# Kernel tuning notes

Measured on AMD Instinct MI355X. Metric: run time of the kernel, lower is better.

## Reference

```python
import jax, jax.numpy as jnp
import numpy as np

N = 200_000        # nodes
E = 2_000_000      # edges (before self loops)
D = 128            # emb_dim
L = 5              # num_layer
NUM_ATOM = 120     # num_atom_type
NUM_CHI = 3        # num_chirality_tag
NUM_BOND = 6       # num_bond_type
NUM_DIR = 3        # num_bond_direction
EPS = 1e-5


def setup_inputs() -> dict:
    key = jax.random.key(0)
    ks = jax.random.split(key, 12)
    s = 0.1
    return {
        "x": jax.random.randint(ks[0], (N, 2), 0, 3, dtype=jnp.int64) if jax.config.jax_enable_x64 else jax.random.randint(ks[0], (N, 2), 0, 3, dtype=jnp.int32),
        "edge_index": jax.random.randint(ks[1], (2, E), 0, N, dtype=jnp.int32),
        "edge_attr": jax.random.randint(ks[2], (E, 2), 0, 3, dtype=jnp.int32),
        "x_emb1": jax.random.normal(ks[3], (NUM_ATOM, D), jnp.float32) * s,
        "x_emb2": jax.random.normal(ks[4], (NUM_CHI, D), jnp.float32) * s,
        "edge_emb1": jax.random.normal(ks[5], (L, NUM_BOND, D), jnp.float32) * s,
        "edge_emb2": jax.random.normal(ks[6], (L, NUM_DIR, D), jnp.float32) * s,
        "w1": jax.random.normal(ks[7], (L, D, 2 * D), jnp.float32) * s,
        "b1": jnp.zeros((L, 2 * D), jnp.float32),
        "w2": jax.random.normal(ks[8], (L, 2 * D, D), jnp.float32) * s,
        "b2": jnp.zeros((L, D), jnp.float32),
        "bn_gamma": jnp.ones((L, D), jnp.float32),
        "bn_beta": jnp.zeros((L, D), jnp.float32),
    }


def reference(x, edge_index, edge_attr, x_emb1, x_emb2, edge_emb1, edge_emb2,
              w1, b1, w2, b2, bn_gamma, bn_beta):
    # node features: atom-type emb + chirality emb
    h = x_emb1[x[:, 0]] + x_emb2[x[:, 1]]                     # [N, D]

    # add self loops; self-loop edge_attr = [4, 0]
    loop = jnp.arange(N, dtype=edge_index.dtype)
    src = jnp.concatenate([edge_index[0], loop])              # [E+N]
    dst = jnp.concatenate([edge_index[1], loop])              # [E+N]
    ea0 = jnp.concatenate([edge_attr[:, 0], jnp.full((N,), 4, edge_attr.dtype)])
    ea1 = jnp.concatenate([edge_attr[:, 1], jnp.zeros((N,), edge_attr.dtype)])

    for l in range(L):
        e_emb = edge_emb1[l][ea0] + edge_emb2[l][ea1]         # [E+N, D]
        msg = h[src] + e_emb                                  # gather + add
        agg = jax.ops.segment_sum(msg, dst, num_segments=N)   # scatter-add
        hid = jax.nn.relu(agg @ w1[l] + b1[l])                # [N, 2D]
        hn = hid @ w2[l] + b2[l]                              # [N, D]
        # BatchNorm1d (training mode, biased variance)
        mean = hn.mean(axis=0)
        var = jnp.mean((hn - mean) ** 2, axis=0)
        hn = bn_gamma[l] * (hn - mean) * jax.lax.rsqrt(var + EPS) + bn_beta[l]
        if l < L - 1:
            hn = jax.nn.relu(hn)
        h = hn
    return h
```

## Files before the change

kernel.cpp:

```cpp
#include <hip/hip_runtime.h>

#define NN 200000
#define NPAD 200192
#define NE 2000000
#define DD 128
#define EPSF 1e-5f

typedef short short4v __attribute__((ext_vector_type(4)));
typedef short short8v __attribute__((ext_vector_type(8)));
typedef float f32x4 __attribute__((ext_vector_type(4)));
typedef float f32x2 __attribute__((ext_vector_type(2)));
typedef unsigned long long u64;

__device__ __forceinline__ ushort f2bf(float f) {
  uint u = __float_as_uint(f);
  uint r = u + 0x7fff + ((u >> 16) & 1);
  return (ushort)(r >> 16);
}
__device__ __forceinline__ float bf2f(ushort u) { return __uint_as_float(((uint)u) << 16); }
__device__ __forceinline__ float bflo(uint v) { return __uint_as_float(v << 16); }
__device__ __forceinline__ float bfhi(uint v) { return __uint_as_float(v & 0xffff0000u); }
__device__ __forceinline__ uint packbf(float a, float b) {
  return (uint)f2bf(a) | ((uint)f2bf(b) << 16);
}

__global__ __launch_bounds__(256) void k_init(const int* __restrict__ x,
    const float* __restrict__ e1, const float* __restrict__ e2,
    uint* __restrict__ h) {
  int t = blockIdx.x * 256 + threadIdx.x;
  if (t >= NN * 64) return;
  int node = t >> 6, cp = (t & 63) << 1;
  int a = x[2 * node], b = x[2 * node + 1];
  float2 va = *(const float2*)(e1 + (size_t)a * DD + cp);
  float2 vb = *(const float2*)(e2 + (size_t)b * DD + cp);
  h[t] = packbf(va.x + vb.x, va.y + vb.y);
}

__global__ __launch_bounds__(256) void k_cvtw(const float* __restrict__ w,
    ushort* __restrict__ wt, int K, int Nc) {
  int t = blockIdx.x * 256 + threadIdx.x;
  if (t >= 5 * K * Nc) return;
  int per = K * Nc;
  int l = t / per, r0 = t % per;
  int j = r0 & 7, lane = (r0 >> 3) & 63, idx = r0 >> 9;
  int KB = K >> 5;
  int kb = idx % KB, ct = idx / KB;
  int lr = lane & 15, qq = lane >> 4;
  int n = ct * 16 + lr;
  int k = kb * 32 + qq * 4 + (j & 3) + ((j >> 2) << 4);
  wt[t] = f2bf(w[(size_t)l * per + (size_t)k * Nc + n]);
}

__global__ __launch_bounds__(256) void k_hist(const int* __restrict__ ei,
    const int* __restrict__ ea, u64* __restrict__ hist8) {
  int e = blockIdx.x * 256 + threadIdx.x;
  if (e >= NE) return;
  int d = ei[NE + e];
  int a0 = ea[2 * e];
  int a1 = ea[2 * e + 1];
  u64 v = (1ull << (a0 * 10)) | (1ull << (30 + a1 * 10));
  atomicAdd(&hist8[(size_t)(blockIdx.x & 7) * NN + d], v);
}

__global__ __launch_bounds__(256) void k_scan1(const u64* __restrict__ hist8,
    u64* __restrict__ histsum, int* __restrict__ off, int* __restrict__ bsum) {
  __shared__ int sh[256];
  int i = blockIdx.x * 256 + threadIdx.x;
  int v = 0;
  if (i < NN) {
    u64 s = 0;
#pragma unroll
    for (int cc = 0; cc < 8; ++cc) s += hist8[(size_t)cc * NN + i];
    histsum[i] = s;
    v = (int)((s & 1023) + ((s >> 10) & 1023) + ((s >> 20) & 1023));
  }
  sh[threadIdx.x] = v;
  __syncthreads();
  for (int d = 1; d < 256; d <<= 1) {
    int xv = 0;
    if (threadIdx.x >= d) xv = sh[threadIdx.x - d];
    __syncthreads();
    if (threadIdx.x >= d) sh[threadIdx.x] += xv;
    __syncthreads();
  }
  if (i < NN) off[i] = sh[threadIdx.x] - v;
  if (threadIdx.x == 255) bsum[blockIdx.x] = sh[255];
}

__global__ __launch_bounds__(1024) void k_scan2(const int* __restrict__ bsum,
    int* __restrict__ boff, int nb) {
  __shared__ int sh[1024];
  int t = threadIdx.x;
  int v = (t < nb) ? bsum[t] : 0;
  sh[t] = v;
  __syncthreads();
  for (int d = 1; d < 1024; d <<= 1) {
    int xv = 0;
    if (t >= d) xv = sh[t - d];
    __syncthreads();
    if (t >= d) sh[t] += xv;
    __syncthreads();
  }
  if (t < nb) boff[t] = sh[t] - v;
}

__global__ __launch_bounds__(256) void k_scan3(int* __restrict__ off,
    const int* __restrict__ boff, const u64* __restrict__ hist8,
    int* __restrict__ cursor8) {
  int i = blockIdx.x * 256 + threadIdx.x;
  if (i < NN) {
    int o = off[i] + boff[i >> 8];
    off[i] = o;
    int run = o;
#pragma unroll
    for (int s = 0; s < 8; ++s) {
      cursor8[(size_t)s * NN + i] = run;
      u64 hs = hist8[(size_t)s * NN + i];
      run += (int)((hs & 1023) + ((hs >> 10) & 1023) + ((hs >> 20) & 1023));
    }
  }
  if (i == 0) off[NN] = NE;
}

__global__ __launch_bounds__(256) void k_scatter(const int* __restrict__ ei,
    int* __restrict__ cursor8, int* __restrict__ csr_src) {
  int e = blockIdx.x * 256 + threadIdx.x;
  if (e >= NE) return;
  int d = ei[NE + e];
  int p = atomicAdd(&cursor8[(size_t)(blockIdx.x & 7) * NN + d], 1);
  csr_src[p] = ei[e];
}

__global__ __launch_bounds__(256) void k_agg(const uint* __restrict__ h,
    uint* __restrict__ agghi, uint* __restrict__ agglo,
    const int* __restrict__ off, const int* __restrict__ src,
    const u64* __restrict__ hist,
    const float* __restrict__ E1, const float* __restrict__ E2) {
  int lane = threadIdx.x & 63;
  int node = blockIdx.x * 4 + (threadIdx.x >> 6);
  int qq = lane >> 4;
  int c = lane & 15;
  f32x2 acc[4];
#pragma unroll
  for (int j = 0; j < 4; ++j) acc[j] = (f32x2){0.f, 0.f};

#define ACCV(V)                                                           \
  {                                                                       \
    acc[0] += (f32x2){bflo(V.x), bfhi(V.x)};                              \
    acc[1] += (f32x2){bflo(V.y), bfhi(V.y)};                              \
    acc[2] += (f32x2){bflo(V.z), bfhi(V.z)};                              \
    acc[3] += (f32x2){bflo(V.w), bfhi(V.w)};                              \
  }

  int beg = off[node], end = off[node + 1];
  int deg = end - beg;
  for (int base = 0; base < deg; base += 64) {
    int nrem = min(deg - base, 64);
    int myidx = 0;
    if (lane < nrem) myidx = src[beg + base + lane];
    int niter = (nrem + 3) >> 2;
    for (int m = 0; m < niter; m += 4) {
      int sl0 = qq + 4 * m;
      int sl1 = sl0 + 4, sl2 = sl0 + 8, sl3 = sl0 + 12;
      int s0 = __shfl(myidx, min(sl0, nrem - 1));
      int s1 = __shfl(myidx, min(sl1, nrem - 1));
      int s2 = __shfl(myidx, min(sl2, nrem - 1));
      int s3 = __shfl(myidx, min(sl3, nrem - 1));
      uint4 v0 = *(const uint4*)(h + (size_t)s0 * 64 + c * 4);
      if (sl0 < nrem) ACCV(v0);
      if (m + 1 < niter) {
        uint4 v1 = *(const uint4*)(h + (size_t)s1 * 64 + c * 4);
        if (sl1 < nrem) ACCV(v1);
      }
      if (m + 2 < niter) {
        uint4 v2 = *(const uint4*)(h + (size_t)s2 * 64 + c * 4);
        if (sl2 < nrem) ACCV(v2);
      }
      if (m + 3 < niter) {
        uint4 v3 = *(const uint4*)(h + (size_t)s3 * 64 + c * 4);
        if (sl3 < nrem) ACCV(v3);
      }
    }
  }
#pragma unroll
  for (int j = 0; j < 4; ++j) {
    acc[j][0] += __shfl_xor(acc[j][0], 16);
    acc[j][1] += __shfl_xor(acc[j][1], 16);
    acc[j][0] += __shfl_xor(acc[j][0], 32);
    acc[j][1] += __shfl_xor(acc[j][1], 32);
  }
  if (lane < 16) {
    uint4 sv = *(const uint4*)(h + (size_t)node * 64 + c * 4);
    ACCV(sv);
    float a[8];
#pragma unroll
    for (int j = 0; j < 4; ++j) { a[2 * j] = acc[j][0]; a[2 * j + 1] = acc[j][1]; }
    u64 hv = hist[node];
    float cnt[7] = {
      (float)(int)(hv & 1023),
      (float)(int)((hv >> 10) & 1023),
      (float)(int)((hv >> 20) & 1023),
      1.f,
      (float)(int)((hv >> 30) & 1023) + 1.f,
      (float)(int)((hv >> 40) & 1023),
      (float)(int)((hv >> 50) & 1023)
    };
    const float* rows[7] = {E1, E1 + DD, E1 + 2 * DD, E1 + 4 * DD,
                            E2, E2 + DD, E2 + 2 * DD};
#pragma unroll
    for (int q = 0; q < 7; ++q) {
      f32x4 e0 = *(const f32x4*)(rows[q] + c * 8);
      f32x4 e1v = *(const f32x4*)(rows[q] + c * 8 + 4);
#pragma unroll
      for (int j = 0; j < 4; ++j) { a[j] += cnt[q] * e0[j]; a[4 + j] += cnt[q] * e1v[j]; }
    }
    int wb = ((c >> 2) << 4) + ((c & 1) << 3) + (((c >> 1) & 1) << 1);
    ushort hA, hB;
    uint2 w01, w23, l01, l23;
    hA = f2bf(a[0]); hB = f2bf(a[1]);
    w01.x = (uint)hA | ((uint)hB << 16);
    l01.x = (uint)f2bf(a[0] - bf2f(hA)) | ((uint)f2bf(a[1] - bf2f(hB)) << 16);
    hA = f2bf(a[2]); hB = f2bf(a[3]);
    w01.y = (uint)hA | ((uint)hB << 16);
    l01.y = (uint)f2bf(a[2] - bf2f(hA)) | ((uint)f2bf(a[3] - bf2f(hB)) << 16);
    hA = f2bf(a[4]); hB = f2bf(a[5]);
    w23.x = (uint)hA | ((uint)hB << 16);
    l23.x = (uint)f2bf(a[4] - bf2f(hA)) | ((uint)f2bf(a[5] - bf2f(hB)) << 16);
    hA = f2bf(a[6]); hB = f2bf(a[7]);
    w23.y = (uint)hA | ((uint)hB << 16);
    l23.y = (uint)f2bf(a[6] - bf2f(hA)) | ((uint)f2bf(a[7] - bf2f(hB)) << 16);
    *(uint2*)(agghi + (size_t)node * 64 + wb) = w01;
    *(uint2*)(agghi + (size_t)node * 64 + wb + 4) = w23;
    *(uint2*)(agglo + (size_t)node * 64 + wb) = l01;
    *(uint2*)(agglo + (size_t)node * 64 + wb + 4) = l23;
  }
#undef ACCV
}

__global__ __launch_bounds__(512, 1) void k_mlp(
    const ushort* __restrict__ agghi, const ushort* __restrict__ agglo,
    const ushort* __restrict__ w1,
    const float* __restrict__ b1,
    const ushort* __restrict__ w2,
    const float* __restrict__ b2, uint* __restrict__ hnb,
    float* __restrict__ bnsums) {
  __shared__ uint4 smem4[8192];
  __shared__ float sstat[256];
  const ushort* sw1 = (const ushort*)smem4;
  const ushort* sw2 = (const ushort*)(smem4 + 4096);
  int t = threadIdx.x;
  int lane = t & 63;
  int wid = t >> 6;
  int nb = blockIdx.x * 256 + wid * 32;
  int lr = lane & 15, qq = lane >> 4;

  if (t < 256) sstat[t] = 0.f;

  short8v afh[2][4], afl[2][4];
#pragma unroll
  for (int g = 0; g < 2; ++g) {
    const ushort* ph = agghi + (size_t)(nb + g * 16 + lr) * 128 + qq * 8;
    const ushort* pl = agglo + (size_t)(nb + g * 16 + lr) * 128 + qq * 8;
#pragma unroll
    for (int kb = 0; kb < 4; ++kb) {
      afh[g][kb] = *(const short8v*)(ph + kb * 32);
      afl[g][kb] = *(const short8v*)(pl + kb * 32);
    }
  }

  {
    const uint4* g1 = (const uint4*)w1;
    const uint4* g2 = (const uint4*)w2;
#pragma unroll
    for (int i = 0; i < 8; ++i) smem4[i * 512 + t] = g1[i * 512 + t];
#pragma unroll
    for (int i = 0; i < 8; ++i) smem4[4096 + i * 512 + t] = g2[i * 512 + t];
  }
  __syncthreads();

  f32x4 acc2[2][8];
#pragma unroll
  for (int g = 0; g < 2; ++g)
#pragma unroll
    for (int ct = 0; ct < 8; ++ct) acc2[g][ct] = (f32x4){0.f, 0.f, 0.f, 0.f};

#pragma unroll
  for (int ph = 0; ph < 4; ++ph) {
    f32x4 acc1[2][4];
#pragma unroll
    for (int g = 0; g < 2; ++g)
#pragma unroll
      for (int ct = 0; ct < 4; ++ct) acc1[g][ct] = (f32x4){0.f, 0.f, 0.f, 0.f};
#pragma unroll
    for (int ct = 0; ct < 4; ++ct) {
      int gct = ph * 4 + ct;
#pragma unroll
      for (int kb = 0; kb < 4; ++kb) {
        short8v wf = *(const short8v*)(sw1 + ((gct * 4 + kb) * 64 + lane) * 8);
        acc1[0][ct] = __builtin_amdgcn_mfma_f32_16x16x32_bf16(wf, afh[0][kb], acc1[0][ct], 0, 0, 0);
        acc1[0][ct] = __builtin_amdgcn_mfma_f32_16x16x32_bf16(wf, afl[0][kb], acc1[0][ct], 0, 0, 0);
        acc1[1][ct] = __builtin_amdgcn_mfma_f32_16x16x32_bf16(wf, afh[1][kb], acc1[1][ct], 0, 0, 0);
        acc1[1][ct] = __builtin_amdgcn_mfma_f32_16x16x32_bf16(wf, afl[1][kb], acc1[1][ct], 0, 0, 0);
      }
    }
    short8v hfh[2][2], hfl[2][2];
#pragma unroll
    for (int i = 0; i < 2; ++i) {
      f32x4 ba = *(const f32x4*)(b1 + (ph * 4 + 2 * i) * 16 + qq * 4);
      f32x4 bb = *(const f32x4*)(b1 + (ph * 4 + 2 * i + 1) * 16 + qq * 4);
#pragma unroll
      for (int g = 0; g < 2; ++g) {
        short8v hh, hl;
#pragma unroll
        for (int r = 0; r < 4; ++r) {
          float va = fmaxf(acc1[g][2 * i][r] + ba[r], 0.f);
          float vb = fmaxf(acc1[g][2 * i + 1][r] + bb[r], 0.f);
          ushort ha = f2bf(va), hb = f2bf(vb);
          hh[r] = (short)ha; hh[4 + r] = (short)hb;
          hl[r] = (short)f2bf(va - bf2f(ha));
          hl[4 + r] = (short)f2bf(vb - bf2f(hb));
        }
        hfh[g][i] = hh; hfl[g][i] = hl;
      }
    }
#pragma unroll
    for (int ct = 0; ct < 8; ++ct) {
#pragma unroll
      for (int i = 0; i < 2; ++i) {
        int kb2 = ph * 2 + i;
        short8v wf = *(const short8v*)(sw2 + ((ct * 8 + kb2) * 64 + lane) * 8);
        acc2[0][ct] = __builtin_amdgcn_mfma_f32_16x16x32_bf16(wf, hfh[0][i], acc2[0][ct], 0, 0, 0);
        acc2[0][ct] = __builtin_amdgcn_mfma_f32_16x16x32_bf16(wf, hfl[0][i], acc2[0][ct], 0, 0, 0);
        acc2[1][ct] = __builtin_amdgcn_mfma_f32_16x16x32_bf16(wf, hfh[1][i], acc2[1][ct], 0, 0, 0);
        acc2[1][ct] = __builtin_amdgcn_mfma_f32_16x16x32_bf16(wf, hfl[1][i], acc2[1][ct], 0, 0, 0);
      }
    }
  }

  int n0 = nb + lr, n1 = nb + 16 + lr;
  float m0 = (n0 < NN) ? 1.f : 0.f;
  float m1 = (n1 < NN) ? 1.f : 0.f;
#pragma unroll
  for (int ct = 0; ct < 8; ++ct) {
    f32x4 bb = *(const f32x4*)(b2 + ct * 16 + qq * 4);
    f32x4 o0, o1;
#pragma unroll
    for (int r = 0; r < 4; ++r) {
      o0[r] = acc2[0][ct][r] + bb[r];
      o1[r] = acc2[1][ct][r] + bb[r];
    }
#pragma unroll
    for (int r = 0; r < 4; ++r) {
      float s = m0 * o0[r] + m1 * o1[r];
      float q = m0 * o0[r] * o0[r] + m1 * o1[r] * o1[r];
      s += __shfl_xor(s, 1); q += __shfl_xor(q, 1);
      s += __shfl_xor(s, 2); q += __shfl_xor(q, 2);
      s += __shfl_xor(s, 4); q += __shfl_xor(q, 4);
      s += __shfl_xor(s, 8); q += __shfl_xor(q, 8);
      if (lr == 0) {
        int col = ct * 16 + qq * 4 + r;
        atomicAdd(&sstat[col], s);
        atomicAdd(&sstat[128 + col], q);
      }
    }
    if (n0 < NN) {
      uint2 wv;
      wv.x = packbf(o0[0], o0[1]);
      wv.y = packbf(o0[2], o0[3]);
      *(uint2*)(hnb + (size_t)n0 * 64 + ct * 8 + qq * 2) = wv;
    }
    if (n1 < NN) {
      uint2 wv;
      wv.x = packbf(o1[0], o1[1]);
      wv.y = packbf(o1[2], o1[3]);
      *(uint2*)(hnb + (size_t)n1 * 64 + ct * 8 + qq * 2) = wv;
    }
  }
  __syncthreads();
  if (t < 256) atomicAdd(&bnsums[t], sstat[t]);
}

__global__ __launch_bounds__(256) void k_bnapply(const uint* __restrict__ hnb,
    const float* __restrict__ sums, const float* __restrict__ gamma,
    const float* __restrict__ beta, uint* __restrict__ hout,
    float* __restrict__ fout, int final_layer) {
  int t = blockIdx.x * 256 + threadIdx.x;
  if (t >= NN * 64) return;
  int node = t >> 6, cp = (t & 63) << 1;
  uint v = hnb[t];
  float r[2] = {bflo(v), bfhi(v)};
#pragma unroll
  for (int j = 0; j < 2; ++j) {
    int col = cp + j;
    float mean = sums[col] * (1.f / NN);
    float var = sums[128 + col] * (1.f / NN) - mean * mean;
    float scale = gamma[col] * rsqrtf(var + EPSF);
    r[j] = (r[j] - mean) * scale + beta[col];
  }
  if (final_layer) {
    *(float2*)(fout + (size_t)node * DD + cp) = make_float2(r[0], r[1]);
  } else {
    hout[t] = packbf(fmaxf(r[0], 0.f), fmaxf(r[1], 0.f));
  }
}

extern "C" void kernel_launch(void* const* d_in, const int* in_sizes, int n_in,
                              void* d_out, int out_size, void* d_ws, size_t ws_size,
                              hipStream_t stream) {
  const int* x    = (const int*)d_in[0];
  const int* ei   = (const int*)d_in[1];
  const int* ea   = (const int*)d_in[2];
  const float* xe1 = (const float*)d_in[3];
  const float* xe2 = (const float*)d_in[4];
  const float* ee1 = (const float*)d_in[5];
  const float* ee2 = (const float*)d_in[6];
  const float* w1  = (const float*)d_in[7];
  const float* b1  = (const float*)d_in[8];
  const float* w2  = (const float*)d_in[9];
  const float* b2  = (const float*)d_in[10];
  const float* gam = (const float*)d_in[11];
  const float* bet = (const float*)d_in[12];
  float* out = (float*)d_out;

  char* p = (char*)d_ws;
  auto alloc = [&](size_t bytes) {
    char* r = p;
    p += (bytes + 255) & ~(size_t)255;
    return r;
  };
  uint* h      = (uint*)alloc((size_t)NN * 64 * 4);
  uint* agghi  = (uint*)alloc((size_t)NPAD * 64 * 4);
  uint* agglo  = (uint*)alloc((size_t)NPAD * 64 * 4);
  uint* hnb    = (uint*)alloc((size_t)NPAD * 64 * 4);
  ushort* w1t  = (ushort*)alloc((size_t)5 * 128 * 256 * 2);
  ushort* w2t  = (ushort*)alloc((size_t)5 * 256 * 128 * 2);
  u64* hist8   = (u64*)alloc((size_t)8 * NN * 8);
  u64* histsum = (u64*)alloc((size_t)NN * 8);
  int* csroff  = (int*)alloc((size_t)(NN + 1) * 4);
  int* cursor8 = (int*)alloc((size_t)8 * NN * 4);
  int* csrsrc  = (int*)alloc((size_t)NE * 4);
  int* bsum    = (int*)alloc(4096);
  int* boff    = (int*)alloc(4096);
  float* bnsums = (float*)alloc(5 * 1024);

  const int nscan = (NN + 255) / 256;

  hipMemsetAsync(hist8, 0, (size_t)8 * NN * 8, stream);
  hipMemsetAsync(bnsums, 0, 5 * 1024, stream);

  k_cvtw<<<(5 * 128 * 256 + 255) / 256, 256, 0, stream>>>(w1, w1t, 128, 256);
  k_cvtw<<<(5 * 256 * 128 + 255) / 256, 256, 0, stream>>>(w2, w2t, 256, 128);
  k_init<<<(NN * 64 + 255) / 256, 256, 0, stream>>>(x, xe1, xe2, h);
  k_hist<<<(NE + 255) / 256, 256, 0, stream>>>(ei, ea, hist8);
  k_scan1<<<nscan, 256, 0, stream>>>(hist8, histsum, csroff, bsum);
  k_scan2<<<1, 1024, 0, stream>>>(bsum, boff, nscan);
  k_scan3<<<nscan, 256, 0, stream>>>(csroff, boff, hist8, cursor8);
  k_scatter<<<(NE + 255) / 256, 256, 0, stream>>>(ei, cursor8, csrsrc);

  for (int l = 0; l < 5; ++l) {
    k_agg<<<NN / 4, 256, 0, stream>>>(h, agghi, agglo, csroff, csrsrc, histsum,
                                      ee1 + (size_t)l * 6 * DD,
                                      ee2 + (size_t)l * 3 * DD);
    k_mlp<<<NPAD / 256, 512, 0, stream>>>((const ushort*)agghi, (const ushort*)agglo,
                                          w1t + (size_t)l * 128 * 256,
                                          b1 + (size_t)l * 256,
                                          w2t + (size_t)l * 256 * 128,
                                          b2 + (size_t)l * DD, hnb,
                                          bnsums + (size_t)l * 256);
    k_bnapply<<<(NN * 64 + 255) / 256, 256, 0, stream>>>(
        hnb, bnsums + (size_t)l * 256, gam + (size_t)l * DD, bet + (size_t)l * DD,
        h, out, l == 4 ? 1 : 0);
  }
}
```

Baseline: 1.656 ms.

## Process two nodes per wavefront in aggregation kernel with split hi/lo stores

The aggregation kernel now gives each 64-lane wavefront two destination nodes, one per 32-lane half, with two 16-lane groups per node instead of four. The aim is to cut the reduction shuffles and to keep more lanes busy through the epilogue, which was previously done by only 16 lanes. The hi and lo bf16 outputs are now written by different sub-groups, spreading the store work. The trade-off is divergence when the two nodes' degrees differ, since the loop runs to the larger degree, and fewer independent loads in flight per node.

```diff
diff --git a/kernel.cpp b/kernel.cpp
--- a/kernel.cpp
+++ b/kernel.cpp
@@ -137,9 +137,19 @@
     const u64* __restrict__ hist,
     const float* __restrict__ E1, const float* __restrict__ E2) {
   int lane = threadIdx.x & 63;
-  int node = blockIdx.x * 4 + (threadIdx.x >> 6);
-  int qq = lane >> 4;
+  int wid = threadIdx.x >> 6;
+  int nb = blockIdx.x * 8 + wid * 2;
+  int half = lane >> 5;
+  int sub = (lane >> 4) & 1;
   int c = lane & 15;
+  int node = nb + half;
+
+  int o0 = off[nb], o1 = off[nb + 1], o2 = off[nb + 2];
+  int deg0 = o1 - o0, deg1 = o2 - o1;
+  int begh = half ? o1 : o0;
+  int degh = half ? deg1 : deg0;
+  int dmax = max(deg0, deg1);
+
   f32x2 acc[4];
 #pragma unroll
   for (int j = 0; j < 4; ++j) acc[j] = (f32x2){0.f, 0.f};
@@ -152,33 +162,25 @@
     acc[3] += (f32x2){bflo(V.w), bfhi(V.w)};                              \
   }
 
-  int beg = off[node], end = off[node + 1];
-  int deg = end - beg;
-  for (int base = 0; base < deg; base += 64) {
-    int nrem = min(deg - base, 64);
+  for (int base = 0; base < dmax; base += 32) {
+    int nremh = degh - base;
+    nremh = nremh < 0 ? 0 : (nremh > 32 ? 32 : nremh);
+    int li = lane & 31;
     int myidx = 0;
-    if (lane < nrem) myidx = src[beg + base + lane];
-    int niter = (nrem + 3) >> 2;
+    if (li < nremh) myidx = src[begh + base + li];
+    int r0 = deg0 - base; r0 = r0 < 0 ? 0 : (r0 > 32 ? 32 : r0);
+    int r1 = deg1 - base; r1 = r1 < 0 ? 0 : (r1 > 32 ? 32 : r1);
+    int niter = (max(r0, r1) + 1) >> 1;
     for (int m = 0; m < niter; m += 4) {
-      int sl0 = qq + 4 * m;
-      int sl1 = sl0 + 4, sl2 = sl0 + 8, sl3 = sl0 + 12;
-      int s0 = __shfl(myidx, min(sl0, nrem - 1));
-      int s1 = __shfl(myidx, min(sl1, nrem - 1));
-      int s2 = __shfl(myidx, min(sl2, nrem - 1));
-      int s3 = __shfl(myidx, min(sl3, nrem - 1));
-      uint4 v0 = *(const uint4*)(h + (size_t)s0 * 64 + c * 4);
-      if (sl0 < nrem) ACCV(v0);
-      if (m + 1 < niter) {
-        uint4 v1 = *(const uint4*)(h + (size_t)s1 * 64 + c * 4);
-        if (sl1 < nrem) ACCV(v1);
-      }
-      if (m + 2 < niter) {
-        uint4 v2 = *(const uint4*)(h + (size_t)s2 * 64 + c * 4);
-        if (sl2 < nrem) ACCV(v2);
-      }
-      if (m + 3 < niter) {
-        uint4 v3 = *(const uint4*)(h + (size_t)s3 * 64 + c * 4);
-        if (sl3 < nrem) ACCV(v3);
+#pragma unroll
+      for (int u = 0; u < 4; ++u) {
+        if (m + u < niter) {
+          int sl = 2 * (m + u) + sub;
+          int srcl = (half << 5) + max(min(sl, nremh - 1), 0);
+          int s = __shfl(myidx, srcl);
+          uint4 v = *(const uint4*)(h + (size_t)s * 64 + c * 4);
+          if (sl < nremh) ACCV(v);
+        }
       }
     }
   }
@@ -186,54 +188,51 @@
   for (int j = 0; j < 4; ++j) {
     acc[j][0] += __shfl_xor(acc[j][0], 16);
     acc[j][1] += __shfl_xor(acc[j][1], 16);
-    acc[j][0] += __shfl_xor(acc[j][0], 32);
-    acc[j][1] += __shfl_xor(acc[j][1], 32);
-  }
-  if (lane < 16) {
-    uint4 sv = *(const uint4*)(h + (size_t)node * 64 + c * 4);
-    ACCV(sv);
-    float a[8];
-#pragma unroll
-    for (int j = 0; j < 4; ++j) { a[2 * j] = acc[j][0]; a[2 * j + 1] = acc[j][1]; }
-    u64 hv = hist[node];
-    float cnt[7] = {
-      (float)(int)(hv & 1023),
-      (float)(int)((hv >> 10) & 1023),
-      (float)(int)((hv >> 20) & 1023),
-      1.f,
-      (float)(int)((hv >> 30) & 1023) + 1.f,
-      (float)(int)((hv >> 40) & 1023),
-      (float)(int)((hv >> 50) & 1023)
-    };
-    const float* rows[7] = {E1, E1 + DD, E1 + 2 * DD, E1 + 4 * DD,
-                            E2, E2 + DD, E2 + 2 * DD};
-#pragma unroll
-    for (int q = 0; q < 7; ++q) {
-      f32x4 e0 = *(const f32x4*)(rows[q] + c * 8);
-      f32x4 e1v = *(const f32x4*)(rows[q] + c * 8 + 4);
-#pragma unroll
-      for (int j = 0; j < 4; ++j) { a[j] += cnt[q] * e0[j]; a[4 + j] += cnt[q] * e1v[j]; }
-    }
-    int wb = ((c >> 2) << 4) + ((c & 1) << 3) + (((c >> 1) & 1) << 1);
-    ushort hA, hB;
-    uint2 w01, w23, l01, l23;
-    hA = f2bf(a[0]); hB = f2bf(a[1]);
-    w01.x = (uint)hA | ((uint)hB << 16);
-    l01.x = (uint)f2bf(a[0] - bf2f(hA)) | ((uint)f2bf(a[1] - bf2f(hB)) << 16);
-    hA = f2bf(a[2]); hB = f2bf(a[3]);
-    w01.y = (uint)hA | ((uint)hB << 16);
-    l01.y = (uint)f2bf(a[2] - bf2f(hA)) | ((uint)f2bf(a[3] - bf2f(hB)) << 16);
-    hA = f2bf(a[4]); hB = f2bf(a[5]);
-    w23.x = (uint)hA | ((uint)hB << 16);
-    l23.x = (uint)f2bf(a[4] - bf2f(hA)) | ((uint)f2bf(a[5] - bf2f(hB)) << 16);
-    hA = f2bf(a[6]); hB = f2bf(a[7]);
-    w23.y = (uint)hA | ((uint)hB << 16);
-    l23.y = (uint)f2bf(a[6] - bf2f(hA)) | ((uint)f2bf(a[7] - bf2f(hB)) << 16);
-    *(uint2*)(agghi + (size_t)node * 64 + wb) = w01;
-    *(uint2*)(agghi + (size_t)node * 64 + wb + 4) = w23;
-    *(uint2*)(agglo + (size_t)node * 64 + wb) = l01;
-    *(uint2*)(agglo + (size_t)node * 64 + wb + 4) = l23;
-  }
+  }
+
+  uint4 sv = *(const uint4*)(h + (size_t)node * 64 + c * 4);
+  ACCV(sv);
+  float a[8];
+#pragma unroll
+  for (int j = 0; j < 4; ++j) { a[2 * j] = acc[j][0]; a[2 * j + 1] = acc[j][1]; }
+  u64 hv = hist[node];
+  float cnt[7] = {
+    (float)(int)(hv & 1023),
+    (float)(int)((hv >> 10) & 1023),
+    (float)(int)((hv >> 20) & 1023),
+    1.f,
+    (float)(int)((hv >> 30) & 1023) + 1.f,
+    (float)(int)((hv >> 40) & 1023),
+    (float)(int)((hv >> 50) & 1023)
+  };
+  const float* rows[7] = {E1, E1 + DD, E1 + 2 * DD, E1 + 4 * DD,
+                          E2, E2 + DD, E2 + 2 * DD};
+#pragma unroll
+  for (int q = 0; q < 7; ++q) {
+    f32x4 e0 = *(const f32x4*)(rows[q] + c * 8);
+    f32x4 e1v = *(const f32x4*)(rows[q] + c * 8 + 4);
+#pragma unroll
+    for (int j = 0; j < 4; ++j) { a[j] += cnt[q] * e0[j]; a[4 + j] += cnt[q] * e1v[j]; }
+  }
+  ushort hbuf[8];
+#pragma unroll
+  for (int j = 0; j < 8; ++j) hbuf[j] = f2bf(a[j]);
+  uint2 v01, v23;
+  if (sub == 0) {
+    v01.x = (uint)hbuf[0] | ((uint)hbuf[1] << 16);
+    v01.y = (uint)hbuf[2] | ((uint)hbuf[3] << 16);
+    v23.x = (uint)hbuf[4] | ((uint)hbuf[5] << 16);
+    v23.y = (uint)hbuf[6] | ((uint)hbuf[7] << 16);
+  } else {
+    v01.x = (uint)f2bf(a[0] - bf2f(hbuf[0])) | ((uint)f2bf(a[1] - bf2f(hbuf[1])) << 16);
+    v01.y = (uint)f2bf(a[2] - bf2f(hbuf[2])) | ((uint)f2bf(a[3] - bf2f(hbuf[3])) << 16);
+    v23.x = (uint)f2bf(a[4] - bf2f(hbuf[4])) | ((uint)f2bf(a[5] - bf2f(hbuf[5])) << 16);
+    v23.y = (uint)f2bf(a[6] - bf2f(hbuf[6])) | ((uint)f2bf(a[7] - bf2f(hbuf[7])) << 16);
+  }
+  uint* dst = sub ? agglo : agghi;
+  int wb = ((c >> 2) << 4) + ((c & 1) << 3) + (((c >> 1) & 1) << 1);
+  *(uint2*)(dst + (size_t)node * 64 + wb) = v01;
+  *(uint2*)(dst + (size_t)node * 64 + wb + 4) = v23;
 #undef ACCV
 }
 
@@ -458,7 +457,7 @@
   k_scatter<<<(NE + 255) / 256, 256, 0, stream>>>(ei, cursor8, csrsrc);
 
   for (int l = 0; l < 5; ++l) {
-    k_agg<<<NN / 4, 256, 0, stream>>>(h, agghi, agglo, csroff, csrsrc, histsum,
+    k_agg<<<NN / 8, 256, 0, stream>>>(h, agghi, agglo, csroff, csrsrc, histsum,
                                       ee1 + (size_t)l * 6 * DD,
                                       ee2 + (size_t)l * 3 * DD);
     k_mlp<<<NPAD / 256, 512, 0, stream>>>((const ushort*)agghi, (const ushort*)agglo,
```

Measured after the change: 1.474 ms (median of 2 runs). -11.0%, faster.
